# Kernel tuning notes

Hardware: AMD Instinct MI355X
Metric: run time of the kernel (lower is better)

The kernel has to match this reference:

```python
import math
import jax, jax.numpy as jnp
import numpy as np

N_EMBD = 1024
N_HEAD = 16
EPS = 1e-5


def get_alibi_slopes(n_head):
    def pow2_slopes(n):
        start = 2 ** (-2 ** (-(math.log2(n) - 3)))
        return [start * start ** i for i in range(n)]
    if math.log2(n_head).is_integer():
        slopes = pow2_slopes(n_head)
    else:
        c = 2 ** math.floor(math.log2(n_head))
        slopes = pow2_slopes(c)
        extra = pow2_slopes(2 * c)[0::2]
        slopes.extend(extra[: n_head - c])
    return jnp.asarray(slopes, dtype=jnp.float32)


def layernorm(x, w, b):
    mu = jnp.mean(x, axis=-1, keepdims=True)
    var = jnp.var(x, axis=-1, keepdims=True)
    return (x - mu) * jax.lax.rsqrt(var + EPS) * w + b


def setup_inputs() -> dict:
    key = jax.random.key(0)
    ks = jax.random.split(key, 8)
    C = N_EMBD
    B, T = 2, 2048
    s = 0.02
    return {
        "x": jax.random.normal(ks[0], (B, T, C), dtype=jnp.float32),
        "ln1_w": jnp.ones((C,), jnp.float32),
        "ln1_b": jnp.zeros((C,), jnp.float32),
        "w_qkv": jax.random.normal(ks[1], (C, 3 * C), dtype=jnp.float32) * s,
        "b_qkv": jnp.zeros((3 * C,), jnp.float32),
        "w_proj": jax.random.normal(ks[2], (C, C), dtype=jnp.float32) * s,
        "b_proj": jnp.zeros((C,), jnp.float32),
        "ln2_w": jnp.ones((C,), jnp.float32),
        "ln2_b": jnp.zeros((C,), jnp.float32),
        "w_fc": jax.random.normal(ks[3], (C, 4 * C), dtype=jnp.float32) * s,
        "b_fc": jnp.zeros((4 * C,), jnp.float32),
        "w_fc2": jax.random.normal(ks[4], (4 * C, C), dtype=jnp.float32) * s,
        "b_fc2": jnp.zeros((C,), jnp.float32),
    }


def reference(x, ln1_w, ln1_b, w_qkv, b_qkv, w_proj, b_proj,
              ln2_w, ln2_b, w_fc, b_fc, w_fc2, b_fc2):
    B, T, C = x.shape
    H = N_HEAD
    D = C // H

    # --- attention with ALiBi ---
    h = layernorm(x, ln1_w, ln1_b)
    qkv = h @ w_qkv + b_qkv                       # [B,T,3C]
    q, k, v = jnp.split(qkv, 3, axis=-1)
    q = q.reshape(B, T, H, D).transpose(0, 2, 1, 3)  # [B,H,T,D]
    k = k.reshape(B, T, H, D).transpose(0, 2, 1, 3)
    v = v.reshape(B, T, H, D).transpose(0, 2, 1, 3)

    att = jnp.einsum('bhqd,bhkd->bhqk', q, k) * (1.0 / math.sqrt(D))

    pos = jnp.arange(T, dtype=jnp.float32)
    distances = pos[:, None] - pos[None, :]        # [T,T], i-j
    slopes = get_alibi_slopes(H)[:, None, None]     # [H,1,1]
    bias = slopes * distances[None, :, :]           # [H,T,T]
    causal = jnp.triu(jnp.ones((T, T), dtype=bool), k=1)
    bias = jnp.where(causal[None, :, :], -jnp.inf, bias)

    att = jax.nn.softmax(att + bias[None], axis=-1)
    y = jnp.einsum('bhqk,bhkd->bhqd', att, v)
    y = y.transpose(0, 2, 1, 3).reshape(B, T, C)
    x = x + y @ w_proj + b_proj

    # --- MLP ---
    h = layernorm(x, ln2_w, ln2_b)
    h = jax.nn.gelu(h @ w_fc + b_fc, approximate=False)
    x = x + h @ w_fc2 + b_fc2
    return x
```

## Files before the change

kernel.cpp:

```cpp
#include <hip/hip_runtime.h>
#include <hip/hip_bf16.h>
#include <math.h>

#define N_EMBD 1024
#define N_HEADC 16
#define HEAD_D 64

typedef __attribute__((ext_vector_type(8))) short short8;
typedef __attribute__((ext_vector_type(4))) float floatx4;

__device__ __forceinline__ ushort f2b(float f) {
    __hip_bfloat16 h = __float2bfloat16(f);
    return *reinterpret_cast<ushort*>(&h);
}

__device__ __forceinline__ void async_cp16(const void* gsrc, void* ldst) {
    __builtin_amdgcn_global_load_lds(
        (const __attribute__((address_space(1))) void*)gsrc,
        (__attribute__((address_space(3))) void*)ldst, 16, 0, 0);
}

__device__ __forceinline__ int xcd_swizzle(int bid, int nwg) {
    const int q = nwg >> 3, r = nwg & 7;
    const int xcd = bid & 7, loc = bid >> 3;
    return (xcd < r ? xcd * (q + 1) : r * (q + 1) + (xcd - r) * q) + loc;
}

template <int CTRL>
__device__ __forceinline__ float dppf(float x) {
    int r = __builtin_amdgcn_update_dpp(0, __builtin_bit_cast(int, x),
                                        CTRL, 0xF, 0xF, true);
    return __builtin_bit_cast(float, r);
}
__device__ __forceinline__ float redmax16(float x) {
    x = fmaxf(x, dppf<0xB1>(x));
    x = fmaxf(x, dppf<0x4E>(x));
    x = fmaxf(x, dppf<0x141>(x));
    x = fmaxf(x, dppf<0x140>(x));
    return x;
}
__device__ __forceinline__ float redsum16(float x) {
    x += dppf<0xB1>(x);
    x += dppf<0x4E>(x);
    x += dppf<0x141>(x);
    x += dppf<0x140>(x);
    return x;
}

__global__ __launch_bounds__(256) void ln_kernel(const float* __restrict__ x,
                                                 const float* __restrict__ w,
                                                 const float* __restrict__ b,
                                                 ushort* __restrict__ out) {
    const int row = blockIdx.x;
    const int t = threadIdx.x;
    const float4 v = reinterpret_cast<const float4*>(x + (size_t)row * N_EMBD)[t];
    float s  = v.x + v.y + v.z + v.w;
    float ss = v.x * v.x + v.y * v.y + v.z * v.z + v.w * v.w;
    for (int o = 32; o > 0; o >>= 1) {
        s  += __shfl_down(s, o);
        ss += __shfl_down(ss, o);
    }
    __shared__ float as_[4], ass_[4];
    const int wid = t >> 6, lane = t & 63;
    if (lane == 0) { as_[wid] = s; ass_[wid] = ss; }
    __syncthreads();
    const float ts  = as_[0] + as_[1] + as_[2] + as_[3];
    const float tss = ass_[0] + ass_[1] + ass_[2] + ass_[3];
    const float mu  = ts * (1.f / N_EMBD);
    const float var = tss * (1.f / N_EMBD) - mu * mu;
    const float inv = rsqrtf(var + 1e-5f);
    const float4 wv = reinterpret_cast<const float4*>(w)[t];
    const float4 bv = reinterpret_cast<const float4*>(b)[t];
    ushort4 o;
    o.x = f2b((v.x - mu) * inv * wv.x + bv.x);
    o.y = f2b((v.y - mu) * inv * wv.y + bv.y);
    o.z = f2b((v.z - mu) * inv * wv.z + bv.z);
    o.w = f2b((v.w - mu) * inv * wv.w + bv.w);
    reinterpret_cast<ushort4*>(out + (size_t)row * N_EMBD)[t] = o;
}

__global__ void convtrans_kernel(const float* __restrict__ W,
                                 ushort* __restrict__ Wt, int K, int N) {
    __shared__ float tile[32][33];
    const int tid = threadIdx.x;
    const int r = tid >> 3;
    const int c4 = (tid & 7) * 4;
    const int bx = blockIdx.x, by = blockIdx.y;

    float4 v = *(const float4*)&W[((size_t)(by * 32 + r)) * N + bx * 32 + c4];
    tile[r][c4 + 0] = v.x; tile[r][c4 + 1] = v.y;
    tile[r][c4 + 2] = v.z; tile[r][c4 + 3] = v.w;
    __syncthreads();

    ushort4 u;
    u.x = f2b(tile[c4 + 0][r]); u.y = f2b(tile[c4 + 1][r]);
    u.z = f2b(tile[c4 + 2][r]); u.w = f2b(tile[c4 + 3][r]);
    *(ushort4*)&Wt[((size_t)(bx * 32 + r)) * K + by * 32 + c4] = u;
}

__device__ __forceinline__ void gemm_stage(
        const ushort* __restrict__ A, const ushort* __restrict__ Bt,
        ushort* As, ushort* Bs,
        int m0, int n0, int K, int k0, int w, int lane) {
#pragma unroll
    for (int l = 0; l < 2; l++) {
        const int cbase = w * 128 + l * 64;
        const int c = cbase + lane;
        const int row = c >> 2, kc8 = (c & 3) * 8;
        async_cp16(A  + (size_t)(m0 + row) * K + k0 + kc8, &As[cbase * 8]);
        async_cp16(Bt + (size_t)(n0 + row) * K + k0 + kc8, &Bs[cbase * 8]);
    }
}

__device__ __forceinline__ void gemm_compute(
        const ushort* As, const ushort* Bs, floatx4 (*acc)[4],
        int wm, int wn, int quad, int l16) {
    short8 a[4], bf[4];
#pragma unroll
    for (int i = 0; i < 4; i++)
        a[i] = *(const short8*)&As[(wm * 64 + i * 16 + l16) * 32 + quad * 8];
#pragma unroll
    for (int j = 0; j < 4; j++)
        bf[j] = *(const short8*)&Bs[(wn * 64 + j * 16 + l16) * 32 + quad * 8];
#pragma unroll
    for (int i = 0; i < 4; i++)
#pragma unroll
        for (int j = 0; j < 4; j++)
            acc[i][j] = __builtin_amdgcn_mfma_f32_16x16x32_bf16(
                a[i], bf[j], acc[i][j], 0, 0, 0);
}

__global__ __launch_bounds__(256) void gemm_bf16_kernel(
        const ushort* __restrict__ A,
        const ushort* __restrict__ Bt,
        const float* __restrict__ bias,
        const float* __restrict__ residual,
        float* __restrict__ out32,
        ushort* __restrict__ out16,
        int M, int N, int K, int do_gelu) {
    __shared__ ushort As[2][128 * 32];
    __shared__ ushort Bs[2][128 * 32];

    const int tid  = threadIdx.x;
    const int w    = tid >> 6;
    const int lane = tid & 63;
    const int quad = lane >> 4;
    const int l16  = lane & 15;
    const int wm   = w >> 1;
    const int wn   = w & 1;

    int bid = blockIdx.y * gridDim.x + blockIdx.x;
    bid = xcd_swizzle(bid, gridDim.x * gridDim.y);
    const int bx = bid % gridDim.x;
    const int by = bid / gridDim.x;
    const int m0 = by * 128;
    const int n0 = bx * 128;

    const int kchunk = K / gridDim.z;
    const int kbeg   = blockIdx.z * kchunk;
    if (gridDim.z > 1)
        out32 += (size_t)blockIdx.z * M * N;

    floatx4 acc[4][4];
#pragma unroll
    for (int i = 0; i < 4; i++)
#pragma unroll
        for (int j = 0; j < 4; j++) acc[i][j] = (floatx4){0.f, 0.f, 0.f, 0.f};

    const int nt = kchunk >> 5;

    gemm_stage(A, Bt, As[0], Bs[0], m0, n0, K, kbeg, w, lane);
    __syncthreads();

    for (int t = 0; t < nt; t += 2) {
        gemm_stage(A, Bt, As[1], Bs[1], m0, n0, K, kbeg + ((t + 1) << 5), w, lane);
        gemm_compute(As[0], Bs[0], acc, wm, wn, quad, l16);
        __syncthreads();
        if (t + 2 < nt)
            gemm_stage(A, Bt, As[0], Bs[0], m0, n0, K, kbeg + ((t + 2) << 5), w, lane);
        gemm_compute(As[1], Bs[1], acc, wm, wn, quad, l16);
        __syncthreads();
    }

#pragma unroll
    for (int i = 0; i < 4; i++) {
#pragma unroll
        for (int j = 0; j < 4; j++) {
            const int nn = n0 + wn * 64 + j * 16 + l16;
            const float bv = bias ? bias[nn] : 0.f;
#pragma unroll
            for (int r = 0; r < 4; r++) {
                const int mm = m0 + wm * 64 + i * 16 + quad * 4 + r;
                float v = acc[i][j][r] + bv;
                if (do_gelu) v = 0.5f * v * (1.f + erff(v * 0.70710678118654752f));
                if (residual) v += residual[(size_t)mm * N + nn];
                if (out32) out32[(size_t)mm * N + nn] = v;
                if (out16) out16[(size_t)mm * N + nn] = f2b(v);
            }
        }
    }
}

__global__ __launch_bounds__(256) void combine_kernel(
        const float* __restrict__ p0, const float* __restrict__ p1,
        const float* __restrict__ bias, float* __restrict__ out) {
    const int i = blockIdx.x * 256 + threadIdx.x;
    const float4 a = ((const float4*)p0)[i];
    const float4 c = ((const float4*)p1)[i];
    const float4 bb = ((const float4*)bias)[i & 255];
    float4 o = ((float4*)out)[i];
    o.x += a.x + c.x + bb.x;
    o.y += a.y + c.y + bb.y;
    o.z += a.z + c.z + bb.z;
    o.w += a.w + c.w + bb.w;
    ((float4*)out)[i] = o;
}

#define AT_PAD 72
#define LOG2E 1.4426950408889634f

__device__ __forceinline__ void attn_tile_step(
        short8 aq0, short8 aq1,
        ushort (*__restrict__ Ks)[AT_PAD],
        ushort (*__restrict__ Vt)[AT_PAD],
        ushort (*__restrict__ Ps)[AT_PAD],
        float* m_r, float* l_r, floatx4* acc,
        int q0, int kt, bool domask,
        float qs2, float slope2, const float* skb,
        int w, int quad, int l16) {
    floatx4 sfrag[4];
#pragma unroll
    for (int kb = 0; kb < 4; kb++) {
        const int kcol = kb * 16 + l16;
        short8 bk0 = *(const short8*)&Ks[kcol][quad * 8];
        short8 bk1 = *(const short8*)&Ks[kcol][32 + quad * 8];
        floatx4 s = (floatx4){0.f, 0.f, 0.f, 0.f};
        s = __builtin_amdgcn_mfma_f32_16x16x32_bf16(aq0, bk0, s, 0, 0, 0);
        s = __builtin_amdgcn_mfma_f32_16x16x32_bf16(aq1, bk1, s, 0, 0, 0);
        sfrag[kb] = s;
    }

    const int psw = ((w * 4 + quad) & 7) << 3;
    int pcol[4];
#pragma unroll
    for (int kb = 0; kb < 4; kb++) pcol[kb] = (kb * 16 + l16) ^ psw;

    const float ktb = (float)(kt * 64);
#pragma unroll
    for (int r = 0; r < 4; r++) {
        const int q = q0 + w * 16 + quad * 4 + r;
        const float rowc = slope2 * ((float)q - ktb);
        float sv[4];
        float rm = -INFINITY;
#pragma unroll
        for (int kb = 0; kb < 4; kb++) {
            float s = fmaf(sfrag[kb][r], qs2, rowc) - skb[kb];
            if (domask) {
                const int k = kt * 64 + kb * 16 + l16;
                s = (k <= q) ? s : -INFINITY;
            }
            sv[kb] = s;
            rm = fmaxf(rm, s);
        }
        rm = redmax16(rm);
        if (rm > m_r[r]) {
            const float corr = exp2f(m_r[r] - rm);
            m_r[r] = rm;
            l_r[r] *= corr;
#pragma unroll
            for (int db = 0; db < 4; db++) acc[db][r] *= corr;
        }
        float rs = 0.f;
#pragma unroll
        for (int kb = 0; kb < 4; kb++) {
            const float pv = exp2f(sv[kb] - m_r[r]);
            rs += pv;
            Ps[w * 16 + quad * 4 + r][pcol[kb]] = f2b(pv);
        }
        rs = redsum16(rs);
        l_r[r] += rs;
    }

    const int prw = ((w * 4 + (l16 >> 2)) & 7) << 3;
    short8 ap0 = *(const short8*)&Ps[w * 16 + l16][(quad * 8) ^ prw];
    short8 ap1 = *(const short8*)&Ps[w * 16 + l16][(32 + quad * 8) ^ prw];
#pragma unroll
    for (int db = 0; db < 4; db++) {
        const int dv = db * 16 + l16;
        const int svw = ((db * 4 + (l16 >> 2)) & 7) << 3;
        short8 bv0 = *(const short8*)&Vt[dv][(quad * 8) ^ svw];
        short8 bv1 = *(const short8*)&Vt[dv][(32 + quad * 8) ^ svw];
        acc[db] = __builtin_amdgcn_mfma_f32_16x16x32_bf16(ap0, bv0, acc[db], 0, 0, 0);
        acc[db] = __builtin_amdgcn_mfma_f32_16x16x32_bf16(ap1, bv1, acc[db], 0, 0, 0);
    }
}

__global__ __launch_bounds__(256) void attn_mfma_kernel(
        const ushort* __restrict__ qkv, ushort* __restrict__ y, int B, int T) {
    const int C3 = 3 * N_EMBD;
    const int NT = T / 64;

    const int gx = gridDim.x, gxy = gridDim.x * gridDim.y;
    int lin = blockIdx.z * gxy + blockIdx.y * gx + blockIdx.x;
    lin = xcd_swizzle(lin, gxy * gridDim.z);
    const int p = lin % gx;
    const int h = (lin / gx) % gridDim.y;
    const int b = lin / gxy;

    const int qt = NT - 1 - p;
    const int tid  = threadIdx.x;
    const int lane = tid & 63;
    const int w    = tid >> 6;
    const int quad = lane >> 4;
    const int l16  = lane & 15;

    __shared__ ushort Qs[64][AT_PAD];
    __shared__ ushort Ks[64][AT_PAD];
    __shared__ ushort Vt[64][AT_PAD];
    __shared__ ushort Ps[64][AT_PAD];

    const float slope  = exp2f(-0.5f * (float)(h + 1));
    const float slope2 = slope * LOG2E;
    const float qs2    = 0.125f * LOG2E;
    float skb[4];
#pragma unroll
    for (int kb = 0; kb < 4; kb++) skb[kb] = slope2 * (float)(kb * 16 + l16);

    const int q0 = qt * 64;
    const size_t hb = (size_t)b * T * C3 + (size_t)h * HEAD_D;

#pragma unroll
    for (int i = 0; i < 4; i++) {
        int idx = tid + i * 256;
        int row = idx >> 4, d0 = (idx & 15) * 4;
        *(ushort4*)&Qs[row][d0] =
            *(const ushort4*)&qkv[hb + (size_t)(q0 + row) * C3 + d0];
    }
    __syncthreads();

    const int mrow = w * 16 + l16;
    short8 aq0 = *(const short8*)&Qs[mrow][quad * 8];
    short8 aq1 = *(const short8*)&Qs[mrow][32 + quad * 8];

    float m_r[4], l_r[4];
    floatx4 acc[4];
#pragma unroll
    for (int r = 0; r < 4; r++) {
        m_r[r] = -INFINITY; l_r[r] = 0.f;
        acc[r] = (floatx4){0.f, 0.f, 0.f, 0.f};
    }

    for (int kt = 0; kt <= qt; kt++) {
#pragma unroll
        for (int i = 0; i < 4; i++) {
            int idx = tid + i * 256;
            int row = idx >> 4, d0 = (idx & 15) * 4;
            const size_t src = hb + (size_t)(kt * 64 + row) * C3 + d0;
            *(ushort4*)&Ks[row][d0] = *(const ushort4*)&qkv[src + N_EMBD];
            ushort4 vv = *(const ushort4*)&qkv[src + 2 * N_EMBD];
            const int rs = row ^ ((idx & 7) << 3);
            Vt[d0 + 0][rs] = vv.x;
            Vt[d0 + 1][rs] = vv.y;
            Vt[d0 + 2][rs] = vv.z;
            Vt[d0 + 3][rs] = vv.w;
        }
        __syncthreads();

        attn_tile_step(aq0, aq1, Ks, Vt, Ps, m_r, l_r, acc,
                       q0, kt, kt == qt, qs2, slope2, skb, w, quad, l16);
        __syncthreads();
    }

#pragma unroll
    for (int r = 0; r < 4; r++) {
        const int qa = q0 + w * 16 + quad * 4 + r;
        const float ia = 1.f / l_r[r];
#pragma unroll
        for (int db = 0; db < 4; db++) {
            y[((size_t)b * T + qa) * N_EMBD + h * HEAD_D + db * 16 + l16] =
                f2b(acc[db][r] * ia);
        }
    }
}

extern "C" void kernel_launch(void* const* d_in, const int* in_sizes, int n_in,
                              void* d_out, int out_size, void* d_ws, size_t ws_size,
                              hipStream_t stream) {
    const int B = 2, T = 2048, C = N_EMBD;
    const int M = B * T;

    const float* x      = (const float*)d_in[0];
    const float* ln1_w  = (const float*)d_in[1];
    const float* ln1_b  = (const float*)d_in[2];
    const float* w_qkv  = (const float*)d_in[3];
    const float* b_qkv  = (const float*)d_in[4];
    const float* w_proj = (const float*)d_in[5];
    const float* b_proj = (const float*)d_in[6];
    const float* ln2_w  = (const float*)d_in[7];
    const float* ln2_b  = (const float*)d_in[8];
    const float* w_fc   = (const float*)d_in[9];
    const float* b_fc   = (const float*)d_in[10];
    const float* w_fc2  = (const float*)d_in[11];
    const float* b_fc2  = (const float*)d_in[12];
    float* out = (float*)d_out;

    char* ws = (char*)d_ws;
    size_t off = 0;
    ushort* wt_qkv  = (ushort*)(ws + off); off += (size_t)3 * C * C * 2;
    ushort* wt_proj = (ushort*)(ws + off); off += (size_t)C * C * 2;
    ushort* wt_fc   = (ushort*)(ws + off); off += (size_t)4 * C * C * 2;
    ushort* wt_fc2  = (ushort*)(ws + off); off += (size_t)4 * C * C * 2;
    ushort* h16     = (ushort*)(ws + off); off += (size_t)M * C * 2;
    ushort* qkv16   = (ushort*)(ws + off); off += (size_t)M * 3 * C * 2;
    ushort* y16     = (ushort*)(ws + off); off += (size_t)M * C * 2;
    ushort* fc16    = (ushort*)(ws + off); off += (size_t)M * 4 * C * 2;

    convtrans_kernel<<<dim3(3 * C / 32, C / 32), 256, 0, stream>>>(w_qkv, wt_qkv, C, 3 * C);
    convtrans_kernel<<<dim3(C / 32, C / 32), 256, 0, stream>>>(w_proj, wt_proj, C, C);
    convtrans_kernel<<<dim3(4 * C / 32, C / 32), 256, 0, stream>>>(w_fc, wt_fc, C, 4 * C);
    convtrans_kernel<<<dim3(C / 32, 4 * C / 32), 256, 0, stream>>>(w_fc2, wt_fc2, 4 * C, C);

    ln_kernel<<<M, 256, 0, stream>>>(x, ln1_w, ln1_b, h16);

    gemm_bf16_kernel<<<dim3(3 * C / 128, M / 128), 256, 0, stream>>>(
        h16, wt_qkv, b_qkv, nullptr, nullptr, qkv16, M, 3 * C, C, 0);

    attn_mfma_kernel<<<dim3(T / 64, N_HEADC, B), 256, 0, stream>>>(
        qkv16, y16, B, T);

    gemm_bf16_kernel<<<dim3(C / 128, M / 128), 256, 0, stream>>>(
        y16, wt_proj, b_proj, x, out, nullptr, M, C, C, 0);

    ln_kernel<<<M, 256, 0, stream>>>(out, ln2_w, ln2_b, h16);

    gemm_bf16_kernel<<<dim3(4 * C / 128, M / 128), 256, 0, stream>>>(
        h16, wt_fc, b_fc, nullptr, nullptr, fc16, M, 4 * C, C, 1);

    float* part = (float*)h16;
    gemm_bf16_kernel<<<dim3(C / 128, M / 128, 2), 256, 0, stream>>>(
        fc16, wt_fc2, nullptr, nullptr, part, nullptr, M, C, 4 * C, 0);
    combine_kernel<<<(M * C) / (256 * 4), 256, 0, stream>>>(
        part, part + (size_t)M * C, b_fc2, out);
}
```

Measured before the change: 440.9 us.

## Prefetch next K/V tile into registers during attention tile compute

Measured after the change: 443.7 us. About the same (+0.6%).

```diff
diff --git a/kernel.cpp b/kernel.cpp
--- a/kernel.cpp
+++ b/kernel.cpp
@@ -314,10 +314,9 @@
     const int quad = lane >> 4;
     const int l16  = lane & 15;
 
-    __shared__ ushort Qs[64][AT_PAD];
+    __shared__ ushort QPs[64][AT_PAD];
     __shared__ ushort Ks[64][AT_PAD];
     __shared__ ushort Vt[64][AT_PAD];
-    __shared__ ushort Ps[64][AT_PAD];
 
     const float slope  = exp2f(-0.5f * (float)(h + 1));
     const float slope2 = slope * LOG2E;
@@ -329,18 +328,25 @@
     const int q0 = qt * 64;
     const size_t hb = (size_t)b * T * C3 + (size_t)h * HEAD_D;
 
+    int srow[4], sd0[4], svr[4];
 #pragma unroll
     for (int i = 0; i < 4; i++) {
-        int idx = tid + i * 256;
-        int row = idx >> 4, d0 = (idx & 15) * 4;
-        *(ushort4*)&Qs[row][d0] =
-            *(const ushort4*)&qkv[hb + (size_t)(q0 + row) * C3 + d0];
+        const int idx = tid + i * 256;
+        srow[i] = idx >> 4;
+        sd0[i]  = (idx & 15) * 4;
+        svr[i]  = srow[i] ^ ((idx & 7) << 3);
+    }
+
+#pragma unroll
+    for (int i = 0; i < 4; i++) {
+        *(ushort4*)&QPs[srow[i]][sd0[i]] =
+            *(const ushort4*)&qkv[hb + (size_t)(q0 + srow[i]) * C3 + sd0[i]];
     }
     __syncthreads();
 
     const int mrow = w * 16 + l16;
-    short8 aq0 = *(const short8*)&Qs[mrow][quad * 8];
-    short8 aq1 = *(const short8*)&Qs[mrow][32 + quad * 8];
+    short8 aq0 = *(const short8*)&QPs[mrow][quad * 8];
+    short8 aq1 = *(const short8*)&QPs[mrow][32 + quad * 8];
 
     float m_r[4], l_r[4];
     floatx4 acc[4];
@@ -350,24 +356,45 @@
         acc[r] = (floatx4){0.f, 0.f, 0.f, 0.f};
     }
 
+#pragma unroll
+    for (int i = 0; i < 4; i++) {
+        const size_t src = hb + (size_t)srow[i] * C3 + sd0[i];
+        *(ushort4*)&Ks[srow[i]][sd0[i]] = *(const ushort4*)&qkv[src + N_EMBD];
+        ushort4 vv = *(const ushort4*)&qkv[src + 2 * N_EMBD];
+        Vt[sd0[i] + 0][svr[i]] = vv.x;
+        Vt[sd0[i] + 1][svr[i]] = vv.y;
+        Vt[sd0[i] + 2][svr[i]] = vv.z;
+        Vt[sd0[i] + 3][svr[i]] = vv.w;
+    }
+    __syncthreads();
+
     for (int kt = 0; kt <= qt; kt++) {
-#pragma unroll
-        for (int i = 0; i < 4; i++) {
-            int idx = tid + i * 256;
-            int row = idx >> 4, d0 = (idx & 15) * 4;
-            const size_t src = hb + (size_t)(kt * 64 + row) * C3 + d0;
-            *(ushort4*)&Ks[row][d0] = *(const ushort4*)&qkv[src + N_EMBD];
-            ushort4 vv = *(const ushort4*)&qkv[src + 2 * N_EMBD];
-            const int rs = row ^ ((idx & 7) << 3);
-            Vt[d0 + 0][rs] = vv.x;
-            Vt[d0 + 1][rs] = vv.y;
-            Vt[d0 + 2][rs] = vv.z;
-            Vt[d0 + 3][rs] = vv.w;
-        }
+        ushort4 kreg[4], vreg[4];
+        const bool pf = (kt < qt);
+        if (pf) {
+#pragma unroll
+            for (int i = 0; i < 4; i++) {
+                const size_t src =
+                    hb + (size_t)((kt + 1) * 64 + srow[i]) * C3 + sd0[i];
+                kreg[i] = *(const ushort4*)&qkv[src + N_EMBD];
+                vreg[i] = *(const ushort4*)&qkv[src + 2 * N_EMBD];
+            }
+        }
+
+        attn_tile_step(aq0, aq1, Ks, Vt, QPs, m_r, l_r, acc,
+                       q0, kt, kt == qt, qs2, slope2, skb, w, quad, l16);
         __syncthreads();
 
-        attn_tile_step(aq0, aq1, Ks, Vt, Ps, m_r, l_r, acc,
-                       q0, kt, kt == qt, qs2, slope2, skb, w, quad, l16);
+        if (pf) {
+#pragma unroll
+            for (int i = 0; i < 4; i++) {
+                *(ushort4*)&Ks[srow[i]][sd0[i]] = kreg[i];
+                Vt[sd0[i] + 0][svr[i]] = vreg[i].x;
+                Vt[sd0[i] + 1][svr[i]] = vreg[i].y;
+                Vt[sd0[i] + 2][svr[i]] = vreg[i].z;
+                Vt[sd0[i] + 3][svr[i]] = vreg[i].w;
+            }
+        }
         __syncthreads();
     }
 
```
